# Kernel tuning notes

Measured on AMD Instinct MI355X. Metric: run time of the kernel, lower is better.

Reference implementation:

```python
import jax, jax.numpy as jnp
import numpy as np

N_EMBD = 1024
N_HEAD = 16


def setup_inputs() -> dict:
    key = jax.random.key(0)
    ks = jax.random.split(key, 5)
    B, T, C = 2, 2048, N_EMBD
    x = jax.random.normal(ks[0], (B, T, C), dtype=jnp.float32)
    # parameters (stored as (in, out); forward uses x @ W + b, equivalent to torch Linear)
    s1 = 1.0 / np.sqrt(C)
    W_attn = jax.random.normal(ks[1], (C, 3 * C), dtype=jnp.float32) * s1
    b_attn = jnp.zeros((3 * C,), dtype=jnp.float32)
    W_proj = jax.random.normal(ks[2], (C, C), dtype=jnp.float32) * s1
    b_proj = jnp.zeros((C,), dtype=jnp.float32)
    return {"x": x, "W_attn": W_attn, "b_attn": b_attn, "W_proj": W_proj, "b_proj": b_proj}


def reference(x, W_attn, b_attn, W_proj, b_proj):
    B, T, C = x.shape
    H = N_HEAD
    D = C // H  # head dim
    qkv = x @ W_attn + b_attn                       # [B, T, 3C]
    q, k, v = jnp.split(qkv, 3, axis=-1)
    # [B, H, T, D]
    q = q.reshape(B, T, H, D).transpose(0, 2, 1, 3)
    k = k.reshape(B, T, H, D).transpose(0, 2, 1, 3)
    v = v.reshape(B, T, H, D).transpose(0, 2, 1, 3)
    scale = 1.0 / jnp.sqrt(jnp.asarray(D, dtype=q.dtype))
    wei = jnp.einsum("bhqd,bhkd->bhqk", q, k) * scale  # [B, H, T, T]
    causal = jnp.tril(jnp.ones((T, T), dtype=bool))
    wei = jnp.where(causal[None, None, :, :], wei, -jnp.inf)
    wei = jax.nn.softmax(wei, axis=-1)
    y = jnp.einsum("bhqk,bhkd->bhqd", wei, v)          # [B, H, T, D]
    y = y.transpose(0, 2, 1, 3).reshape(B, T, C)
    return y @ W_proj + b_proj
```

## Files before the change

### kernel.cpp

```cpp
#include <hip/hip_runtime.h>
#include <hip/hip_bf16.h>

typedef __attribute__((ext_vector_type(8))) short short8;
typedef __attribute__((ext_vector_type(4))) float floatx4;
typedef __attribute__((ext_vector_type(4))) unsigned int uintx4;
#define BF16 __hip_bfloat16

__device__ __forceinline__ unsigned short f2bf(float f) {
  unsigned int u = __builtin_bit_cast(unsigned int, f);
  unsigned int r = (u + 0x7FFFu + ((u >> 16) & 1u)) >> 16;
  return (unsigned short)r;
}

__device__ __forceinline__ unsigned int cvt_pk_bf16(float lo, float hi) {
  unsigned int r;
  asm("v_cvt_pk_bf16_f32 %0, %1, %2" : "=v"(r) : "v"(lo), "v"(hi));
  return r;
}

__device__ __forceinline__ void gload_lds16(const void* g, void* l) {
  __builtin_amdgcn_global_load_lds(
      (const __attribute__((address_space(1))) unsigned int*)g,
      (__attribute__((address_space(3))) unsigned int*)l, 16, 0, 0);
}

__global__ __launch_bounds__(256)
void cvt_bf16(const float* __restrict__ in, unsigned short* __restrict__ out, int n) {
  int i = (blockIdx.x * 256 + threadIdx.x) * 8;
  if (i >= n) return;
  float4 a = *(const float4*)(in + i);
  float4 b = *(const float4*)(in + i + 4);
  short8 v;
  v[0] = (short)f2bf(a.x); v[1] = (short)f2bf(a.y);
  v[2] = (short)f2bf(a.z); v[3] = (short)f2bf(a.w);
  v[4] = (short)f2bf(b.x); v[5] = (short)f2bf(b.y);
  v[6] = (short)f2bf(b.z); v[7] = (short)f2bf(b.w);
  *(short8*)(out + i) = v;
}

__global__ __launch_bounds__(256)
void transpose_cvt(const float* __restrict__ in, unsigned short* __restrict__ out,
                   int K, int N) {
  __shared__ float tile[64][65];
  const int nb = N >> 6;
  const int tn = blockIdx.x % nb, tk = blockIdx.x / nb;
  const int n0 = tn << 6, k0 = tk << 6;
  const int tid = threadIdx.x;
#pragma unroll
  for (int c = 0; c < 4; ++c) {
    int t = tid + c * 256;
    int r = t >> 4, col = (t & 15) << 2;
    float4 v = *(const float4*)(in + (size_t)(k0 + r) * N + n0 + col);
    tile[r][col] = v.x; tile[r][col + 1] = v.y;
    tile[r][col + 2] = v.z; tile[r][col + 3] = v.w;
  }
  __syncthreads();
#pragma unroll
  for (int c = 0; c < 2; ++c) {
    int t = tid + c * 256;
    int r = t >> 3, col = (t & 7) << 3;
    short8 v;
#pragma unroll
    for (int j = 0; j < 8; ++j) v[j] = (short)f2bf(tile[col + j][r]);
    *(short8*)(out + (size_t)(n0 + r) * K + k0 + col) = v;
  }
}

template <int EPI>
__global__ __launch_bounds__(256, 2)
void gemm_bt(const BF16* __restrict__ A, const BF16* __restrict__ Bt,
             const float* __restrict__ bias, void* __restrict__ outv,
             int M, int N, int K) {
  const int tid = threadIdx.x;
  const int w = tid >> 6, l = tid & 63;
  const int lr = l & 15, lg = l >> 4;
  const int nbx = N >> 7;
  const int bm = blockIdx.x / nbx, bn = blockIdx.x % nbx;
  const int row0 = bm << 7, col0 = bn << 7;
  const int wr = (w >> 1) << 6, wc = (w & 1) << 6;

  __shared__ __align__(16) BF16 ldsA[128 * 64];
  __shared__ __align__(16) BF16 ldsB[128 * 64];

  floatx4 acc[4][4] = {};
  const int swzl = (lr & 7) << 3;

  for (int k0 = 0; k0 < K; k0 += 64) {
#pragma unroll
    for (int c = 0; c < 4; ++c) {
      int t = w * 64 + l + c * 256;
      int ar = t >> 3;
      int ch = (t & 7) ^ (ar & 7);
      gload_lds16(A + (size_t)(row0 + ar) * K + k0 + (ch << 3),
                  ldsA + w * 512 + c * 2048);
      gload_lds16(Bt + (size_t)(col0 + ar) * K + k0 + (ch << 3),
                  ldsB + w * 512 + c * 2048);
    }
    __syncthreads();
#pragma unroll
    for (int kk = 0; kk < 64; kk += 32) {
      short8 af[4], bf[4];
#pragma unroll
      for (int m = 0; m < 4; ++m)
        af[m] = *(const short8*)(ldsA + (wr + m * 16 + lr) * 64 + ((kk + lg * 8) ^ swzl));
#pragma unroll
      for (int n = 0; n < 4; ++n)
        bf[n] = *(const short8*)(ldsB + (wc + n * 16 + lr) * 64 + ((kk + lg * 8) ^ swzl));
#pragma unroll
      for (int m = 0; m < 4; ++m)
#pragma unroll
        for (int n = 0; n < 4; ++n)
          acc[m][n] = __builtin_amdgcn_mfma_f32_16x16x32_bf16(af[m], bf[n], acc[m][n], 0, 0, 0);
    }
    __syncthreads();
  }

#pragma unroll
  for (int m = 0; m < 4; ++m)
#pragma unroll
    for (int n = 0; n < 4; ++n)
#pragma unroll
      for (int j = 0; j < 4; ++j) {
        int row = row0 + wr + m * 16 + lg * 4 + j;
        int col = col0 + wc + n * 16 + lr;
        float v = acc[m][n][j] + bias[col];
        if (EPI == 0) {
          BF16* out = (BF16*)outv;
          int s = col >> 10, cc = col & 1023;
          int hh = cc >> 6, dd = cc & 63;
          int bb = row >> 11, tt = row & 2047;
          size_t addr;
          if (s == 2)
            addr = (size_t)8388608 + (((size_t)bb * 16 + hh) * 64 + dd) * 2048 + tt;
          else
            addr = (size_t)s * 4194304 + (((size_t)bb * 16 + hh) * 2048 + tt) * 64 + dd;
          out[addr] = __float2bfloat16(v);
        } else {
          float* out = (float*)outv;
          out[(size_t)row * N + col] = v;
        }
      }
}

__global__ __launch_bounds__(256, 5)
void flash_attn(const BF16* __restrict__ qkv, float* __restrict__ PO,
                float* __restrict__ PL) {
  const int T = 2048;
  const int bid = blockIdx.x;
  const int J = bid >> 5;
  const int bh = bid & 31;
  const int qt = 31 - (J >> 1);
  const int par = J & 1;
  const int q0 = qt << 6;
  const int n = qt + 1;
  const int iters = (n - par + 1) >> 1;
  const int tid = threadIdx.x, w = tid >> 6, l = tid & 63;
  const int lr = l & 15, lg = l >> 4;

  const BF16* Q  = qkv + (size_t)bh * (T * 64);
  const BF16* Kp = qkv + 4194304 + (size_t)bh * (T * 64);
  const BF16* Vt = qkv + 8388608 + (size_t)bh * (64 * T);

  __shared__ __align__(16) BF16 ldsK[2][4096];
  __shared__ __align__(16) BF16 ldsV[2][4096];

  const float C1 = 0.18033688011112042f;
  const float C2 = 17.312340490667562f;
  const int swzl = (lr & 7) << 3;

  short8 qf[2];
#pragma unroll
  for (int c = 0; c < 2; ++c)
    qf[c] = *(const short8*)(Q + (size_t)(q0 + w * 16 + lr) * 64 + c * 32 + lg * 8);

  floatx4 acc_o[4] = {};
  floatx4 lsum4 = {0.f, 0.f, 0.f, 0.f};

  const int t0 = w * 64 + l, t1 = t0 + 256;
  const int r0 = t0 >> 3, ch0 = (t0 & 7) ^ (r0 & 7);
  const int r1 = t1 >> 3, ch1 = (t1 & 7) ^ (r1 & 7);
  const BF16* kg0 = Kp + (((size_t)(par * 64 + r0)) << 6) + ch0 * 8;
  const BF16* kg1 = Kp + (((size_t)(par * 64 + r1)) << 6) + ch1 * 8;
  const BF16* vg0 = Vt + (size_t)r0 * T + par * 64 + ch0 * 8;
  const BF16* vg1 = Vt + (size_t)r1 * T + par * 64 + ch1 * 8;

#define STAGE2(BUF)                                           \
  {                                                           \
    gload_lds16(kg0, &ldsK[BUF][w * 512]);                    \
    gload_lds16(vg0, &ldsV[BUF][w * 512]);                    \
    gload_lds16(kg1, &ldsK[BUF][w * 512 + 2048]);             \
    gload_lds16(vg1, &ldsV[BUF][w * 512 + 2048]);             \
    kg0 += 8192; kg1 += 8192; vg0 += 128; vg1 += 128;         \
  }

#define TILE(IT, MASKED)                                                      \
  {                                                                           \
    const int cur_ = (IT) & 1;                                                \
    if ((IT) + 1 < iters) {                                                   \
      STAGE2(cur_ ^ 1);                                                       \
      asm volatile("s_waitcnt vmcnt(4)" ::: "memory");                        \
    } else {                                                                  \
      asm volatile("s_waitcnt vmcnt(0)" ::: "memory");                        \
    }                                                                         \
    __builtin_amdgcn_s_barrier();                                             \
    floatx4 accs[4] = {};                                                     \
    __builtin_amdgcn_s_setprio(1);                                            \
    _Pragma("unroll")                                                         \
    for (int c = 0; c < 2; ++c)                                               \
      _Pragma("unroll")                                                       \
      for (int n4 = 0; n4 < 4; ++n4) {                                        \
        short8 kf = *(const short8*)(&ldsK[cur_][(n4 * 16 + lr) * 64 +        \
                                                ((c * 32 + lg * 8) ^ swzl)]); \
        accs[n4] = __builtin_amdgcn_mfma_f32_16x16x32_bf16(kf, qf[c], accs[n4], 0, 0, 0); \
      }                                                                       \
    __builtin_amdgcn_s_setprio(0);                                            \
    _Pragma("unroll")                                                         \
    for (int n4 = 0; n4 < 4; ++n4)                                            \
      _Pragma("unroll")                                                       \
      for (int j = 0; j < 4; ++j) {                                           \
        float p = exp2f(fmaf(accs[n4][j], C1, -C2));                          \
        if (MASKED && (n4 * 16 + lg * 4 + j > w * 16 + lr)) p = 0.f;          \
        lsum4[j] += p;                                                        \
        accs[n4][j] = p;                                                      \
      }                                                                       \
    __builtin_amdgcn_s_setprio(1);                                            \
    _Pragma("unroll")                                                         \
    for (int c = 0; c < 2; ++c) {                                             \
      unsigned int a0 = cvt_pk_bf16(accs[2 * c][0], accs[2 * c][1]);          \
      unsigned int b0 = cvt_pk_bf16(accs[2 * c + 1][0], accs[2 * c + 1][1]);  \
      unsigned int a1 = cvt_pk_bf16(accs[2 * c][2], accs[2 * c][3]);          \
      unsigned int b1 = cvt_pk_bf16(accs[2 * c + 1][2], accs[2 * c + 1][3]);  \
      asm("v_permlane32_swap_b32 %0, %1" : "+v"(a0), "+v"(b0));               \
      asm("v_permlane32_swap_b32 %0, %1" : "+v"(a1), "+v"(b1));               \
      asm("v_permlane16_swap_b32 %0, %1" : "+v"(a0), "+v"(b0));               \
      asm("v_permlane16_swap_b32 %0, %1" : "+v"(a1), "+v"(b1));               \
      uintx4 pw; pw[0] = a0; pw[1] = a1; pw[2] = b0; pw[3] = b1;              \
      short8 pf = __builtin_bit_cast(short8, pw);                             \
      _Pragma("unroll")                                                       \
      for (int n4 = 0; n4 < 4; ++n4) {                                        \
        short8 vf = *(const short8*)(&ldsV[cur_][(n4 * 16 + lr) * 64 +        \
                                                ((c * 32 + lg * 8) ^ swzl)]); \
        acc_o[n4] = __builtin_amdgcn_mfma_f32_16x16x32_bf16(pf, vf, acc_o[n4], 0, 0, 0); \
      }                                                                       \
    }                                                                         \
    __builtin_amdgcn_s_setprio(0);                                            \
    __builtin_amdgcn_s_barrier();                                             \
  }

  const int full = iters - ((par == (qt & 1)) ? 1 : 0);
  if (iters > 0) {
    STAGE2(0);
    for (int it = 0; it < full; ++it) TILE(it, false);
    if (full < iters) TILE(full, true);
  }
#undef TILE
#undef STAGE2

  const int slot = (bh * 32 + qt) * 2 + par;
  float lsum = (lsum4[0] + lsum4[1]) + (lsum4[2] + lsum4[3]);
  lsum += __shfl_xor(lsum, 16, 64);
  lsum += __shfl_xor(lsum, 32, 64);
  if (lg == 0) PL[slot * 64 + w * 16 + lr] = lsum;
  float* po = PO + (size_t)slot * 4096;
#pragma unroll
  for (int n4 = 0; n4 < 4; ++n4)
#pragma unroll
    for (int j = 0; j < 4; ++j)
      po[(w * 16 + lg * 4 + j) * 64 + n4 * 16 + lr] = acc_o[n4][j];
}

__global__ __launch_bounds__(256)
void attn_merge(const float* __restrict__ PO, const float* __restrict__ PL,
                BF16* __restrict__ y) {
  const int g = blockIdx.x * 256 + threadIdx.x;
  const int qi = g >> 9;
  const int rem = (g & 511) << 3;
  const int r = rem >> 6, d0 = rem & 63;
  const float* A = PO + (size_t)qi * 8192 + rem;
  const float* B = A + 4096;
  const float lA = PL[qi * 128 + r];
  const float lB = PL[qi * 128 + 64 + r];
  const float inv = 1.0f / (lA + lB);
  float4 a0 = *(const float4*)A, a1 = *(const float4*)(A + 4);
  float4 b0 = *(const float4*)B, b1 = *(const float4*)(B + 4);
  const int bh = qi >> 5, qt = qi & 31;
  const int b = bh >> 4, h = bh & 15;
  const int t = qt * 64 + r;
  short8 v;
  v[0] = (short)f2bf((a0.x + b0.x) * inv);
  v[1] = (short)f2bf((a0.y + b0.y) * inv);
  v[2] = (short)f2bf((a0.z + b0.z) * inv);
  v[3] = (short)f2bf((a0.w + b0.w) * inv);
  v[4] = (short)f2bf((a1.x + b1.x) * inv);
  v[5] = (short)f2bf((a1.y + b1.y) * inv);
  v[6] = (short)f2bf((a1.z + b1.z) * inv);
  v[7] = (short)f2bf((a1.w + b1.w) * inv);
  *(short8*)(y + ((size_t)b * 2048 + t) * 1024 + h * 64 + d0) = v;
}

extern "C" void kernel_launch(void* const* d_in, const int* in_sizes, int n_in,
                              void* d_out, int out_size, void* d_ws, size_t ws_size,
                              hipStream_t stream) {
  const float* x      = (const float*)d_in[0];
  const float* W_attn = (const float*)d_in[1];
  const float* b_attn = (const float*)d_in[2];
  const float* W_proj = (const float*)d_in[3];
  const float* b_proj = (const float*)d_in[4];
  float* out = (float*)d_out;
  BF16* ws  = (BF16*)d_ws;

  BF16* xb      = ws;
  BF16* wt_attn = xb + 4194304;
  BF16* wt_proj = wt_attn + 3145728;
  BF16* qkv     = wt_proj + 1048576;
  BF16* y       = qkv + 12582912;
  float* PO     = (float*)(y + 4194304);
  float* PL     = PO + 8388608;

  hipLaunchKernelGGL(cvt_bf16, dim3(2048), dim3(256), 0, stream,
                     x, (unsigned short*)xb, 4194304);
  hipLaunchKernelGGL(transpose_cvt, dim3(48 * 16), dim3(256), 0, stream,
                     W_attn, (unsigned short*)wt_attn, 1024, 3072);
  hipLaunchKernelGGL(transpose_cvt, dim3(16 * 16), dim3(256), 0, stream,
                     W_proj, (unsigned short*)wt_proj, 1024, 1024);
  hipLaunchKernelGGL(gemm_bt<0>, dim3(32 * 24), dim3(256), 0, stream,
                     xb, wt_attn, b_attn, (void*)qkv, 4096, 3072, 1024);
  hipLaunchKernelGGL(flash_attn, dim3(2048), dim3(256), 0, stream, qkv, PO, PL);
  hipLaunchKernelGGL(attn_merge, dim3(2048), dim3(256), 0, stream, PO, PL, y);
  hipLaunchKernelGGL(gemm_bt<1>, dim3(32 * 8), dim3(256), 0, stream,
                     y, wt_proj, b_proj, (void*)out, 4096, 1024, 1024);
}
```

Baseline: 113.4 us.

## Double-buffer LDS tiles in bf16 GEMM to overlap global loads with MFMA

Adds a second LDS buffer for the A and B tiles in the GEMM kernel. The next K-tile is now prefetched with global_load_lds while the current tile is being multiplied, using a partial vmcnt wait. The aim is to hide global memory latency behind MFMA work. LDS use doubles to 64KB per block, which may reduce occupancy below the launch-bounds target of 2 blocks per CU. The hand-written waitcnt and barrier placement also risks a race: the trailing barrier may not keep a fast wave from overwriting the buffer another wave is still reading.

```diff
diff --git a/kernel.cpp b/kernel.cpp
--- a/kernel.cpp
+++ b/kernel.cpp
@@ -79,41 +79,58 @@
   const int row0 = bm << 7, col0 = bn << 7;
   const int wr = (w >> 1) << 6, wc = (w & 1) << 6;
 
-  __shared__ __align__(16) BF16 ldsA[128 * 64];
-  __shared__ __align__(16) BF16 ldsB[128 * 64];
+  __shared__ __align__(16) BF16 ldsA[2][128 * 64];
+  __shared__ __align__(16) BF16 ldsB[2][128 * 64];
 
   floatx4 acc[4][4] = {};
   const int swzl = (lr & 7) << 3;
 
-  for (int k0 = 0; k0 < K; k0 += 64) {
-#pragma unroll
-    for (int c = 0; c < 4; ++c) {
-      int t = w * 64 + l + c * 256;
-      int ar = t >> 3;
-      int ch = (t & 7) ^ (ar & 7);
-      gload_lds16(A + (size_t)(row0 + ar) * K + k0 + (ch << 3),
-                  ldsA + w * 512 + c * 2048);
-      gload_lds16(Bt + (size_t)(col0 + ar) * K + k0 + (ch << 3),
-                  ldsB + w * 512 + c * 2048);
+  const int NT = K >> 6;
+
+#define GSTAGE(K0, BUF)                                                       \
+  {                                                                           \
+    _Pragma("unroll")                                                         \
+    for (int c = 0; c < 4; ++c) {                                             \
+      int t = w * 64 + l + c * 256;        \
+      int ar = t >> 3;                                                        \
+      int ch = (t & 7) ^ (ar & 7);             \
+      gload_lds16(A + (size_t)(row0 + ar) * K + (K0) + (ch << 3),             \
+                  &ldsA[BUF][w * 512 + c * 2048]);                            \
+      gload_lds16(Bt + (size_t)(col0 + ar) * K + (K0) + (ch << 3),            \
+                  &ldsB[BUF][w * 512 + c * 2048]);                            \
+    }                                                                         \
+  }
+
+  GSTAGE(0, 0);
+
+  for (int kt = 0; kt < NT; ++kt) {
+    const int cur = kt & 1;
+    if (kt + 1 < NT) {
+      GSTAGE((kt + 1) << 6, cur ^ 1);
+      asm volatile("s_waitcnt vmcnt(8)" ::: "memory");
+    } else {
+      asm volatile("s_waitcnt vmcnt(0)" ::: "memory");
     }
-    __syncthreads();
+    __builtin_amdgcn_s_barrier();
+
 #pragma unroll
     for (int kk = 0; kk < 64; kk += 32) {
       short8 af[4], bf[4];
 #pragma unroll
       for (int m = 0; m < 4; ++m)
-        af[m] = *(const short8*)(ldsA + (wr + m * 16 + lr) * 64 + ((kk + lg * 8) ^ swzl));
+        af[m] = *(const short8*)(&ldsA[cur][(wr + m * 16 + lr) * 64 + ((kk + lg * 8) ^ swzl)]);
 #pragma unroll
       for (int n = 0; n < 4; ++n)
-        bf[n] = *(const short8*)(ldsB + (wc + n * 16 + lr) * 64 + ((kk + lg * 8) ^ swzl));
+        bf[n] = *(const short8*)(&ldsB[cur][(wc + n * 16 + lr) * 64 + ((kk + lg * 8) ^ swzl)]);
 #pragma unroll
       for (int m = 0; m < 4; ++m)
 #pragma unroll
         for (int n = 0; n < 4; ++n)
           acc[m][n] = __builtin_amdgcn_mfma_f32_16x16x32_bf16(af[m], bf[n], acc[m][n], 0, 0, 0);
     }
-    __syncthreads();
-  }
+    if (kt + 1 < NT) __builtin_amdgcn_s_barrier();
+  }
+#undef GSTAGE
 
 #pragma unroll
   for (int m = 0; m < 4; ++m)
```

Result: slower. 131.0 us (+15.5%).

## Add double-buffered 128x192 tiled QKV GEMM with 512-thread blocks

Applied to the files above, without the earlier changes.

Replaces the generic templated GEMM for the QKV projection with a dedicated kernel. It uses 128x192 tiles so the grid is 512 blocks of 512 threads (8 waves), which matches the 256-CU count better than 768 blocks. It also double-buffers LDS with async global-to-LDS loads and partial vmcnt waits to overlap loads with MFMA. The cost is more LDS per block (80KB), which may limit occupancy, and a 3-wide N fragment per wave gives lower MFMA reuse per LDS read.

```diff
diff --git a/kernel.cpp b/kernel.cpp
--- a/kernel.cpp
+++ b/kernel.cpp
@@ -66,11 +66,102 @@
   }
 }
 
-template <int EPI>
+__global__ __launch_bounds__(512, 4)
+void gemm_qkv(const BF16* __restrict__ A, const BF16* __restrict__ Bt,
+              const float* __restrict__ bias, BF16* __restrict__ out,
+              int M, int N, int K) {
+  const int tid = threadIdx.x;
+  const int w = tid >> 6, l = tid & 63;
+  const int lr = l & 15, lg = l >> 4;
+  const int bm = blockIdx.x >> 4, bn = blockIdx.x & 15;
+  const int row0 = bm << 7;
+  const int col0 = bn * 192;
+  const int wr = (w >> 2) << 6;
+  const int wc = (w & 3) * 48;
+
+  __shared__ __align__(16) BF16 ldsA[2][128 * 64];
+  __shared__ __align__(16) BF16 ldsB[2][192 * 64];
+
+  floatx4 acc[4][3] = {};
+  const int swzl = (lr & 7) << 3;
+
+#define QSTAGE(K0, BUF)                                                       \
+  {                                                                           \
+    _Pragma("unroll")                                                         \
+    for (int c = 0; c < 2; ++c) {                  \
+      int t = w * 64 + l + c * 512;                                           \
+      int ar = t >> 3;                                                        \
+      int ch = (t & 7) ^ (ar & 7);                                            \
+      gload_lds16(A + (size_t)(row0 + ar) * K + (K0) + (ch << 3),             \
+                  &ldsA[BUF][w * 512 + c * 4096]);                            \
+    }                                                                         \
+    _Pragma("unroll")                                                         \
+    for (int c = 0; c < 3; ++c) {                  \
+      int t = w * 64 + l + c * 512;                                           \
+      int br = t >> 3;                                                        \
+      int ch = (t & 7) ^ (br & 7);                                            \
+      gload_lds16(Bt + (size_t)(col0 + br) * K + (K0) + (ch << 3),            \
+                  &ldsB[BUF][w * 512 + c * 4096]);                            \
+    }                                                                         \
+  }
+
+  const int NT = K >> 6;
+  QSTAGE(0, 0);
+
+  for (int kt = 0; kt < NT; ++kt) {
+    const int cur = kt & 1;
+    if (kt + 1 < NT) {
+      QSTAGE((kt + 1) << 6, cur ^ 1);
+      asm volatile("s_waitcnt vmcnt(5)" ::: "memory");
+    } else {
+      asm volatile("s_waitcnt vmcnt(0)" ::: "memory");
+    }
+    __builtin_amdgcn_s_barrier();
+
+#pragma unroll
+    for (int kk = 0; kk < 64; kk += 32) {
+      short8 af[4], bf[3];
+#pragma unroll
+      for (int m = 0; m < 4; ++m)
+        af[m] = *(const short8*)(&ldsA[cur][(wr + m * 16 + lr) * 64 + ((kk + lg * 8) ^ swzl)]);
+#pragma unroll
+      for (int n = 0; n < 3; ++n)
+        bf[n] = *(const short8*)(&ldsB[cur][(wc + n * 16 + lr) * 64 + ((kk + lg * 8) ^ swzl)]);
+#pragma unroll
+      for (int m = 0; m < 4; ++m)
+#pragma unroll
+        for (int n = 0; n < 3; ++n)
+          acc[m][n] = __builtin_amdgcn_mfma_f32_16x16x32_bf16(af[m], bf[n], acc[m][n], 0, 0, 0);
+    }
+    if (kt + 1 < NT) __builtin_amdgcn_s_barrier();
+  }
+#undef QSTAGE
+
+#pragma unroll
+  for (int m = 0; m < 4; ++m)
+#pragma unroll
+    for (int n = 0; n < 3; ++n)
+#pragma unroll
+      for (int j = 0; j < 4; ++j) {
+        int row = row0 + wr + m * 16 + lg * 4 + j;
+        int col = col0 + wc + n * 16 + lr;
+        float v = acc[m][n][j] + bias[col];
+        int s = col >> 10, cc = col & 1023;
+        int hh = cc >> 6, dd = cc & 63;
+        int bb = row >> 11, tt = row & 2047;
+        size_t addr;
+        if (s == 2)
+          addr = (size_t)8388608 + (((size_t)bb * 16 + hh) * 64 + dd) * 2048 + tt;
+        else
+          addr = (size_t)s * 4194304 + (((size_t)bb * 16 + hh) * 2048 + tt) * 64 + dd;
+        out[addr] = __float2bfloat16(v);
+      }
+}
+
 __global__ __launch_bounds__(256, 2)
-void gemm_bt(const BF16* __restrict__ A, const BF16* __restrict__ Bt,
-             const float* __restrict__ bias, void* __restrict__ outv,
-             int M, int N, int K) {
+void gemm_proj(const BF16* __restrict__ A, const BF16* __restrict__ Bt,
+               const float* __restrict__ bias, float* __restrict__ out,
+               int M, int N, int K) {
   const int tid = threadIdx.x;
   const int w = tid >> 6, l = tid & 63;
   const int lr = l & 15, lg = l >> 4;
@@ -123,22 +214,7 @@
       for (int j = 0; j < 4; ++j) {
         int row = row0 + wr + m * 16 + lg * 4 + j;
         int col = col0 + wc + n * 16 + lr;
-        float v = acc[m][n][j] + bias[col];
-        if (EPI == 0) {
-          BF16* out = (BF16*)outv;
-          int s = col >> 10, cc = col & 1023;
-          int hh = cc >> 6, dd = cc & 63;
-          int bb = row >> 11, tt = row & 2047;
-          size_t addr;
-          if (s == 2)
-            addr = (size_t)8388608 + (((size_t)bb * 16 + hh) * 64 + dd) * 2048 + tt;
-          else
-            addr = (size_t)s * 4194304 + (((size_t)bb * 16 + hh) * 2048 + tt) * 64 + dd;
-          out[addr] = __float2bfloat16(v);
-        } else {
-          float* out = (float*)outv;
-          out[(size_t)row * N + col] = v;
-        }
+        out[(size_t)row * N + col] = acc[m][n][j] + bias[col];
       }
 }
 
@@ -323,10 +399,10 @@
                      W_attn, (unsigned short*)wt_attn, 1024, 3072);
   hipLaunchKernelGGL(transpose_cvt, dim3(16 * 16), dim3(256), 0, stream,
                      W_proj, (unsigned short*)wt_proj, 1024, 1024);
-  hipLaunchKernelGGL(gemm_bt<0>, dim3(32 * 24), dim3(256), 0, stream,
-                     xb, wt_attn, b_attn, (void*)qkv, 4096, 3072, 1024);
+  hipLaunchKernelGGL(gemm_qkv, dim3(512), dim3(512), 0, stream,
+                     xb, wt_attn, b_attn, qkv, 4096, 3072, 1024);
   hipLaunchKernelGGL(flash_attn, dim3(2048), dim3(256), 0, stream, qkv, PO, PL);
   hipLaunchKernelGGL(attn_merge, dim3(2048), dim3(256), 0, stream, PO, PL, y);
-  hipLaunchKernelGGL(gemm_bt<1>, dim3(32 * 8), dim3(256), 0, stream,
-                     y, wt_proj, b_proj, (void*)out, 4096, 1024, 1024);
-}
+  hipLaunchKernelGGL(gemm_proj, dim3(32 * 8), dim3(256), 0, stream,
+                     y, wt_proj, b_proj, out, 4096, 1024, 1024);
+}
```

Measured after the change: 124.5 us. 9.7% more time.

## Drop split-KV attention and merge kernel; normalize and write output directly

Applied to the files above, without the earlier changes.

Each attention block now walks all key tiles for its query tile instead of splitting the keys into two parity halves. That lets it normalize by the row sum and write bf16 y directly, which removes the fp32 partial-output buffers and the separate merge kernel. Blocks are remapped so that each XCD handles a fixed set of heads and long and short query tiles are paired for load balance. The cost is half as many blocks with longer serial loops, plus a lower occupancy bound and a larger V shared buffer that is never used.

```diff
diff --git a/kernel.cpp b/kernel.cpp
--- a/kernel.cpp
+++ b/kernel.cpp
@@ -142,31 +142,32 @@
       }
 }
 
-__global__ __launch_bounds__(256, 5)
-void flash_attn(const BF16* __restrict__ qkv, float* __restrict__ PO,
-                float* __restrict__ PL) {
+__global__ __launch_bounds__(256, 4)
+void flash_attn(const BF16* __restrict__ qkv, BF16* __restrict__ y) {
   const int T = 2048;
-  const int bid = blockIdx.x;
-  const int J = bid >> 5;
-  const int bh = bid & 31;
-  const int qt = 31 - (J >> 1);
-  const int par = J & 1;
+  const int i = blockIdx.x;
+  const int xcd = i & 7, s = i >> 3;
+  const int par = (s ^ (s >> 5)) & 1;
+  const int rnk = ((s >> 5) << 4) | ((s & 31) >> 1);
+  const int bh = xcd * 4 + (rnk & 3);
+  const int hq = rnk >> 2;
+  const int qt = par ? hq : (31 - hq);
+  const int b = bh >> 4, h = bh & 15;
   const int q0 = qt << 6;
-  const int n = qt + 1;
-  const int iters = (n - par + 1) >> 1;
   const int tid = threadIdx.x, w = tid >> 6, l = tid & 63;
   const int lr = l & 15, lg = l >> 4;
 
-  const BF16* Q  = qkv + (size_t)bh * (T * 64);
-  const BF16* Kp = qkv + 4194304 + (size_t)bh * (T * 64);
-  const BF16* Vt = qkv + 8388608 + (size_t)bh * (64 * T);
+  const BF16* Q  = qkv + (size_t)bh * T * 64;
+  const BF16* Kp = qkv + 4194304 + (size_t)bh * T * 64;
+  const BF16* Vt = qkv + 8388608 + (size_t)bh * 64 * T;
 
   __shared__ __align__(16) BF16 ldsK[2][4096];
-  __shared__ __align__(16) BF16 ldsV[2][4096];
+  __shared__ __align__(16) BF16 ldsV[2][6144];
 
   const float C1 = 0.18033688011112042f;
   const float C2 = 17.312340490667562f;
   const int swzl = (lr & 7) << 3;
+  const int nt = qt + 1;
 
   short8 qf[2];
 #pragma unroll
@@ -179,10 +180,10 @@
   const int t0 = w * 64 + l, t1 = t0 + 256;
   const int r0 = t0 >> 3, ch0 = (t0 & 7) ^ (r0 & 7);
   const int r1 = t1 >> 3, ch1 = (t1 & 7) ^ (r1 & 7);
-  const BF16* kg0 = Kp + (((size_t)(par * 64 + r0)) << 6) + ch0 * 8;
-  const BF16* kg1 = Kp + (((size_t)(par * 64 + r1)) << 6) + ch1 * 8;
-  const BF16* vg0 = Vt + (size_t)r0 * T + par * 64 + ch0 * 8;
-  const BF16* vg1 = Vt + (size_t)r1 * T + par * 64 + ch1 * 8;
+  const BF16* kg0 = Kp + ((size_t)r0 << 6) + ch0 * 8;
+  const BF16* kg1 = Kp + ((size_t)r1 << 6) + ch1 * 8;
+  const BF16* vg0 = Vt + (size_t)r0 * T + ch0 * 8;
+  const BF16* vg1 = Vt + (size_t)r1 * T + ch1 * 8;
 
 #define STAGE2(BUF)                                           \
   {                                                           \
@@ -190,19 +191,20 @@
     gload_lds16(vg0, &ldsV[BUF][w * 512]);                    \
     gload_lds16(kg1, &ldsK[BUF][w * 512 + 2048]);             \
     gload_lds16(vg1, &ldsV[BUF][w * 512 + 2048]);             \
-    kg0 += 8192; kg1 += 8192; vg0 += 128; vg1 += 128;         \
+    kg0 += 4096; kg1 += 4096; vg0 += 64; vg1 += 64;           \
   }
 
 #define TILE(IT, MASKED)                                                      \
   {                                                                           \
     const int cur_ = (IT) & 1;                                                \
-    if ((IT) + 1 < iters) {                                                   \
+    if ((IT) + 1 < nt) {                                                      \
       STAGE2(cur_ ^ 1);                                                       \
-      asm volatile("s_waitcnt vmcnt(4)" ::: "memory");                        \
+      asm volatile("s_waitcnt vmcnt(4)" ::: "memory");    \
     } else {                                                                  \
       asm volatile("s_waitcnt vmcnt(0)" ::: "memory");                        \
     }                                                                         \
     __builtin_amdgcn_s_barrier();                                             \
+                   \
     floatx4 accs[4] = {};                                                     \
     __builtin_amdgcn_s_setprio(1);                                            \
     _Pragma("unroll")                                                         \
@@ -214,6 +216,7 @@
         accs[n4] = __builtin_amdgcn_mfma_f32_16x16x32_bf16(kf, qf[c], accs[n4], 0, 0, 0); \
       }                                                                       \
     __builtin_amdgcn_s_setprio(0);                                            \
+                                          \
     _Pragma("unroll")                                                         \
     for (int n4 = 0; n4 < 4; ++n4)                                            \
       _Pragma("unroll")                                                       \
@@ -223,6 +226,7 @@
         lsum4[j] += p;                                                        \
         accs[n4][j] = p;                                                      \
       }                                                                       \
+          \
     __builtin_amdgcn_s_setprio(1);                                            \
     _Pragma("unroll")                                                         \
     for (int c = 0; c < 2; ++c) {                                             \
@@ -247,55 +251,28 @@
     __builtin_amdgcn_s_barrier();                                             \
   }
 
-  const int full = iters - ((par == (qt & 1)) ? 1 : 0);
-  if (iters > 0) {
-    STAGE2(0);
-    for (int it = 0; it < full; ++it) TILE(it, false);
-    if (full < iters) TILE(full, true);
-  }
+  STAGE2(0);
+  for (int it = 0; it < nt - 1; ++it) TILE(it, false);
+  TILE(nt - 1, true);
 #undef TILE
 #undef STAGE2
 
-  const int slot = (bh * 32 + qt) * 2 + par;
   float lsum = (lsum4[0] + lsum4[1]) + (lsum4[2] + lsum4[3]);
   lsum += __shfl_xor(lsum, 16, 64);
   lsum += __shfl_xor(lsum, 32, 64);
-  if (lg == 0) PL[slot * 64 + w * 16 + lr] = lsum;
-  float* po = PO + (size_t)slot * 4096;
+  float inv_own = 1.0f / lsum;
+  float inv[4];
+#pragma unroll
+  for (int j = 0; j < 4; ++j) inv[j] = __shfl(inv_own, lg * 4 + j, 64);
 #pragma unroll
   for (int n4 = 0; n4 < 4; ++n4)
 #pragma unroll
-    for (int j = 0; j < 4; ++j)
-      po[(w * 16 + lg * 4 + j) * 64 + n4 * 16 + lr] = acc_o[n4][j];
-}
-
-__global__ __launch_bounds__(256)
-void attn_merge(const float* __restrict__ PO, const float* __restrict__ PL,
-                BF16* __restrict__ y) {
-  const int g = blockIdx.x * 256 + threadIdx.x;
-  const int qi = g >> 9;
-  const int rem = (g & 511) << 3;
-  const int r = rem >> 6, d0 = rem & 63;
-  const float* A = PO + (size_t)qi * 8192 + rem;
-  const float* B = A + 4096;
-  const float lA = PL[qi * 128 + r];
-  const float lB = PL[qi * 128 + 64 + r];
-  const float inv = 1.0f / (lA + lB);
-  float4 a0 = *(const float4*)A, a1 = *(const float4*)(A + 4);
-  float4 b0 = *(const float4*)B, b1 = *(const float4*)(B + 4);
-  const int bh = qi >> 5, qt = qi & 31;
-  const int b = bh >> 4, h = bh & 15;
-  const int t = qt * 64 + r;
-  short8 v;
-  v[0] = (short)f2bf((a0.x + b0.x) * inv);
-  v[1] = (short)f2bf((a0.y + b0.y) * inv);
-  v[2] = (short)f2bf((a0.z + b0.z) * inv);
-  v[3] = (short)f2bf((a0.w + b0.w) * inv);
-  v[4] = (short)f2bf((a1.x + b1.x) * inv);
-  v[5] = (short)f2bf((a1.y + b1.y) * inv);
-  v[6] = (short)f2bf((a1.z + b1.z) * inv);
-  v[7] = (short)f2bf((a1.w + b1.w) * inv);
-  *(short8*)(y + ((size_t)b * 2048 + t) * 1024 + h * 64 + d0) = v;
+    for (int j = 0; j < 4; ++j) {
+      int qr = q0 + w * 16 + lg * 4 + j;
+      int dd = n4 * 16 + lr;
+      y[((size_t)b * 2048 + qr) * 1024 + h * 64 + dd] =
+          __float2bfloat16(acc_o[n4][j] * inv[j]);
+    }
 }
 
 extern "C" void kernel_launch(void* const* d_in, const int* in_sizes, int n_in,
@@ -314,8 +291,6 @@
   BF16* wt_proj = wt_attn + 3145728;
   BF16* qkv     = wt_proj + 1048576;
   BF16* y       = qkv + 12582912;
-  float* PO     = (float*)(y + 4194304);
-  float* PL     = PO + 8388608;
 
   hipLaunchKernelGGL(cvt_bf16, dim3(2048), dim3(256), 0, stream,
                      x, (unsigned short*)xb, 4194304);
@@ -325,8 +300,7 @@
                      W_proj, (unsigned short*)wt_proj, 1024, 1024);
   hipLaunchKernelGGL(gemm_bt<0>, dim3(32 * 24), dim3(256), 0, stream,
                      xb, wt_attn, b_attn, (void*)qkv, 4096, 3072, 1024);
-  hipLaunchKernelGGL(flash_attn, dim3(2048), dim3(256), 0, stream, qkv, PO, PL);
-  hipLaunchKernelGGL(attn_merge, dim3(2048), dim3(256), 0, stream, PO, PL, y);
+  hipLaunchKernelGGL(flash_attn, dim3(1024), dim3(256), 0, stream, qkv, y);
   hipLaunchKernelGGL(gemm_bt<1>, dim3(32 * 8), dim3(256), 0, stream,
                      y, wt_proj, b_proj, (void*)out, 4096, 1024, 1024);
 }
```

Result: faster. 109.6 us (-3.4%).
